# Kernel optimization log

Hardware: AMD Instinct MI355X
Metric: run time of the kernel (lower is better)

Reference implementation:

```python
import jax, jax.numpy as jnp
import numpy as np

B, T = 8192, 2048


def setup_inputs() -> dict:
    key = jax.random.key(0)
    u = jax.random.normal(key, (B, T, 1), dtype=jnp.float32)
    return {
        "u": u,
        "dt": jnp.float32(0.01),
        "m": jnp.float32(1.0),
        "c": jnp.float32(0.1),
        "k": jnp.float32(2.0),
        "in_mean": jnp.float32(0.5),
        "in_std": jnp.float32(2.0),
        "out_mean": jnp.float32(0.0),
        "out_std": jnp.float32(1.5),
    }


def reference(u, dt, m, c, k, in_mean, in_std, out_mean, out_std):
    # u: (B, T, 1) scaled forcing signal; state: (B, 2) = [position, velocity]
    Bsz = u.shape[0]
    u_seq = jnp.transpose(u[..., 0])  # (T, B) for lax.scan over time
    state0 = jnp.zeros((Bsz, 2), dtype=u.dtype)

    def step(state, u_t):
        # in_s.inverse_transform: unscale input
        u_p = u_t * in_std + in_mean  # (B,)
        x, v = state[:, 0], state[:, 1]
        # prior(state, u_p): mass-spring-damper derivative [dx, dv]
        acc = (u_p - c * v - k * x) / m
        new_state = state + dt * jnp.stack([v, acc], axis=1)  # Euler step
        # prior.ay on the UPDATED state (matches torch: state updated first)
        ay = (u_p - c * new_state[:, 1] - k * new_state[:, 0]) / m
        # out_s.transform: scale output
        y = (ay - out_mean) / out_std  # (B,)
        return new_state, y

    state_T, ys = jax.lax.scan(step, state0, u_seq)  # ys: (T, B)
    return jnp.transpose(ys), state_T  # (B, T), (B, 2)
```

## Files before the change

### kernel.cpp

```cpp
#include <hip/hip_runtime.h>

#define TT 2048

__device__ __forceinline__ float b2f(unsigned short h) {
    union { unsigned int u; float f; } x; x.u = ((unsigned int)h) << 16; return x.f;
}
__device__ __forceinline__ unsigned short f2b(float f) {
    union { float f; unsigned int u; } x; x.f = f;
    unsigned int r = x.u + 0x7fffu + ((x.u >> 16) & 1u);
    return (unsigned short)(r >> 16);
}
__device__ __forceinline__ float ldsc(const void* p, bool bf) {
    return bf ? b2f(*(const unsigned short*)p) : *(const float*)p;
}
__device__ __forceinline__ int swz(int u) { return u ^ ((u >> 3) & 7); }

__device__ __forceinline__ void gload16(const void* g, void* lds_base) {
    __builtin_amdgcn_global_load_lds(
        (const __attribute__((address_space(1))) void*)g,
        (__attribute__((address_space(3))) void*)lds_base,
        16, 0, 0);
}

template<bool BF>
__device__ __forceinline__ void issue_row_loads(const void* u_in, int r, int lane, uint4* Wb) {
    constexpr int NLD = BF ? 4 : 8;
    constexpr int ES  = BF ? 2 : 4;
    const char* g = (const char*)u_in + (size_t)r * TT * ES;
    #pragma unroll
    for (int j = 0; j < NLD; j++)
        gload16(g + (size_t)swz(j * 64 + lane) * 16, (char*)Wb + j * 1024);
}

template<bool BF>
__device__ void run_wave(
    const void* __restrict__ u_in, void* __restrict__ out,
    int rows, int row0, int stride, int lane,
    uint4* __restrict__ U0, uint4* __restrict__ U1,
    float dt, float cc, float kk, float inv_m,
    float im, float is, float om, float inv_os)
{
    constexpr int NLD = BF ? 4 : 8;
    constexpr int ES  = BF ? 2 : 4;

    const float a21 = -dt * kk * inv_m;
    const float a22 = 1.0f - dt * cc * inv_m;
    const float dtm = dt * inv_m;

    issue_row_loads<BF>(u_in, row0, lane, U0);

    int p = 0;
    bool first = true;
    for (int r = row0; r < rows; r += stride) {
        uint4* W  = p ? U1 : U0;
        uint4* Wn = p ? U0 : U1;

        if (first)      { asm volatile("s_waitcnt vmcnt(0)" ::: "memory"); }
        else if (BF)    { asm volatile("s_waitcnt vmcnt(5)" ::: "memory"); }
        else            { asm volatile("s_waitcnt vmcnt(9)" ::: "memory"); }
        __builtin_amdgcn_sched_barrier(0);

        const int rn = r + stride;
        if (rn < rows) issue_row_loads<BF>(u_in, rn, lane, Wn);
        __builtin_amdgcn_sched_barrier(0);

        float uf[32];
        if (BF) {
            #pragma unroll
            for (int m = 0; m < 4; m++) {
                uint4 w = W[swz(lane * 4 + m)];
                unsigned int ws[4] = {w.x, w.y, w.z, w.w};
                #pragma unroll
                for (int q = 0; q < 4; q++) {
                    uf[m*8 + q*2 + 0] = b2f((unsigned short)(ws[q] & 0xffffu));
                    uf[m*8 + q*2 + 1] = b2f((unsigned short)(ws[q] >> 16));
                }
            }
        } else {
            #pragma unroll
            for (int m = 0; m < 8; m++) {
                uint4 w = W[swz(lane * 8 + m)];
                uf[m*4+0] = __uint_as_float(w.x);
                uf[m*4+1] = __uint_as_float(w.y);
                uf[m*4+2] = __uint_as_float(w.z);
                uf[m*4+3] = __uint_as_float(w.w);
            }
        }

        float px = 0.f, pv = 0.f;
        #pragma unroll
        for (int i = 0; i < 32; i++) {
            float up = uf[i] * is + im;
            uf[i] = up;
            float nx = px + dt * pv;
            float nv = a21 * px + a22 * pv + dtm * up;
            px = nx; pv = nv;
        }

        float m00 = 1.f, m01 = dt, m10 = a21, m11 = a22;
        #pragma unroll
        for (int i = 0; i < 5; i++) {
            float t00 = m00*m00 + m01*m10;
            float t01 = m00*m01 + m01*m11;
            float t10 = m10*m00 + m11*m10;
            float t11 = m10*m01 + m11*m11;
            m00=t00; m01=t01; m10=t10; m11=t11;
        }

        #pragma unroll
        for (int o = 1; o < 64; o <<= 1) {
            float rx = __shfl_up(px, o, 64);
            float rv = __shfl_up(pv, o, 64);
            if (lane >= o) {
                px = m00*rx + m01*rv + px;
                pv = m10*rx + m11*rv + pv;
            }
            if (o < 32) {
                float t00 = m00*m00 + m01*m10;
                float t01 = m00*m01 + m01*m11;
                float t10 = m10*m00 + m11*m10;
                float t11 = m10*m01 + m11*m11;
                m00=t00; m01=t01; m10=t10; m11=t11;
            }
        }

        float ex = __shfl_up(px, 1, 64);
        float ev = __shfl_up(pv, 1, 64);
        if (lane == 0) { ex = 0.f; ev = 0.f; }

        float x = ex, v = ev;
        #pragma unroll
        for (int i = 0; i < 32; i++) {
            float up = uf[i];
            float nx = x + dt * v;
            float nv = a21 * x + a22 * v + dtm * up;
            float ay = (up - cc * nv - kk * nx) * inv_m;
            uf[i] = (ay - om) * inv_os;
            x = nx; v = nv;
        }

        if (BF) {
            #pragma unroll
            for (int m = 0; m < 4; m++) {
                uint4 w;
                w.x = (unsigned)f2b(uf[m*8+0]) | ((unsigned)f2b(uf[m*8+1]) << 16);
                w.y = (unsigned)f2b(uf[m*8+2]) | ((unsigned)f2b(uf[m*8+3]) << 16);
                w.z = (unsigned)f2b(uf[m*8+4]) | ((unsigned)f2b(uf[m*8+5]) << 16);
                w.w = (unsigned)f2b(uf[m*8+6]) | ((unsigned)f2b(uf[m*8+7]) << 16);
                W[swz(lane * 4 + m)] = w;
            }
        } else {
            #pragma unroll
            for (int m = 0; m < 8; m++) {
                uint4 w;
                w.x = __float_as_uint(uf[m*4+0]);
                w.y = __float_as_uint(uf[m*4+1]);
                w.z = __float_as_uint(uf[m*4+2]);
                w.w = __float_as_uint(uf[m*4+3]);
                W[swz(lane * 8 + m)] = w;
            }
        }
        __builtin_amdgcn_wave_barrier();

        {
            uint4* g = (uint4*)((char*)out + (size_t)r * TT * ES);
            #pragma unroll
            for (int j = 0; j < NLD; j++) g[j * 64 + lane] = W[swz(j * 64 + lane)];
        }
        if (lane == 63) {
            if (BF) {
                unsigned short* ob = (unsigned short*)out;
                size_t so = (size_t)rows * TT + (size_t)r * 2;
                *(unsigned int*)(ob + so) =
                    (unsigned)f2b(px) | ((unsigned)f2b(pv) << 16);
            } else {
                float* of = (float*)out;
                size_t so = (size_t)rows * TT + (size_t)r * 2;
                *(float2*)(of + so) = make_float2(px, pv);
            }
        }

        p ^= 1;
        first = false;
    }
}

__global__ __launch_bounds__(128, 2) void phys_scan(
    const void* __restrict__ u_in,
    const void* __restrict__ p_dt, const void* __restrict__ p_m,
    const void* __restrict__ p_c,  const void* __restrict__ p_k,
    const void* __restrict__ p_im, const void* __restrict__ p_is,
    const void* __restrict__ p_om, const void* __restrict__ p_os,
    void* __restrict__ out, int rows, int stride)
{
    __shared__ uint4 smem[2][2][512];
    const int lane = threadIdx.x & 63;
    const int wid  = threadIdx.x >> 6;
    const int row0 = blockIdx.x * 2 + wid;
    if (row0 >= rows) return;

    const bool bf = (((const unsigned short*)p_m)[0] != 0);

    const float dt = ldsc(p_dt, bf);
    const float mm = ldsc(p_m,  bf);
    const float cc = ldsc(p_c,  bf);
    const float kk = ldsc(p_k,  bf);
    const float im = ldsc(p_im, bf);
    const float is = ldsc(p_is, bf);
    const float om = ldsc(p_om, bf);
    const float os = ldsc(p_os, bf);
    const float inv_m  = 1.0f / mm;
    const float inv_os = 1.0f / os;

    if (bf) run_wave<true >(u_in, out, rows, row0, stride, lane,
                            smem[wid][0], smem[wid][1],
                            dt, cc, kk, inv_m, im, is, om, inv_os);
    else    run_wave<false>(u_in, out, rows, row0, stride, lane,
                            smem[wid][0], smem[wid][1],
                            dt, cc, kk, inv_m, im, is, om, inv_os);
}

extern "C" void kernel_launch(void* const* d_in, const int* in_sizes, int n_in,
                              void* d_out, int out_size, void* d_ws, size_t ws_size,
                              hipStream_t stream) {
    const int rows = in_sizes[0] / TT;
    int blocks = (rows + 1) / 2;
    if (blocks > 1024) blocks = 1024;
    const int stride = blocks * 2;
    hipLaunchKernelGGL(phys_scan, dim3(blocks), dim3(128), 0, stream,
                       d_in[0], d_in[1], d_in[2], d_in[3], d_in[4],
                       d_in[5], d_in[6], d_in[7], d_in[8],
                       d_out, rows, stride);
}
```

Before: 126.6 us.

## Prefetch rows into registers with a single LDS buffer and double the grid

Replaces the direct global-to-LDS async loads and the LDS double buffer with a register prefetch of the next row. That row is written into one swizzled LDS buffer at the start of each iteration. Halving LDS use allows launch bounds of 4 blocks per CU, and the launcher now allows up to 2048 blocks, so each wave handles fewer rows and more waves run concurrently. The trade-off is extra VGPRs for the prefetch registers. The hardcoded vmcnt waits also no longer match the new load pattern, so the compiler's own waits must preserve ordering.

```diff
diff --git a/kernel.cpp b/kernel.cpp
--- a/kernel.cpp
+++ b/kernel.cpp
@@ -15,28 +15,11 @@
 }
 __device__ __forceinline__ int swz(int u) { return u ^ ((u >> 3) & 7); }
 
-__device__ __forceinline__ void gload16(const void* g, void* lds_base) {
-    __builtin_amdgcn_global_load_lds(
-        (const __attribute__((address_space(1))) void*)g,
-        (__attribute__((address_space(3))) void*)lds_base,
-        16, 0, 0);
-}
-
-template<bool BF>
-__device__ __forceinline__ void issue_row_loads(const void* u_in, int r, int lane, uint4* Wb) {
-    constexpr int NLD = BF ? 4 : 8;
-    constexpr int ES  = BF ? 2 : 4;
-    const char* g = (const char*)u_in + (size_t)r * TT * ES;
-    #pragma unroll
-    for (int j = 0; j < NLD; j++)
-        gload16(g + (size_t)swz(j * 64 + lane) * 16, (char*)Wb + j * 1024);
-}
-
 template<bool BF>
 __device__ void run_wave(
     const void* __restrict__ u_in, void* __restrict__ out,
     int rows, int row0, int stride, int lane,
-    uint4* __restrict__ U0, uint4* __restrict__ U1,
+    uint4* __restrict__ W,
     float dt, float cc, float kk, float inv_m,
     float im, float is, float om, float inv_os)
 {
@@ -47,21 +30,29 @@
     const float a22 = 1.0f - dt * cc * inv_m;
     const float dtm = dt * inv_m;
 
-    issue_row_loads<BF>(u_in, row0, lane, U0);
-
-    int p = 0;
+    uint4 pf[NLD];
+    {
+        const uint4* g = (const uint4*)((const char*)u_in + (size_t)row0 * TT * ES);
+        #pragma unroll
+        for (int j = 0; j < NLD; j++) pf[j] = g[j * 64 + lane];
+    }
+
     bool first = true;
     for (int r = row0; r < rows; r += stride) {
-        uint4* W  = p ? U1 : U0;
-        uint4* Wn = p ? U0 : U1;
-
         if (first)      { asm volatile("s_waitcnt vmcnt(0)" ::: "memory"); }
         else if (BF)    { asm volatile("s_waitcnt vmcnt(5)" ::: "memory"); }
         else            { asm volatile("s_waitcnt vmcnt(9)" ::: "memory"); }
         __builtin_amdgcn_sched_barrier(0);
 
+        #pragma unroll
+        for (int j = 0; j < NLD; j++) W[swz(j * 64 + lane)] = pf[j];
+
         const int rn = r + stride;
-        if (rn < rows) issue_row_loads<BF>(u_in, rn, lane, Wn);
+        if (rn < rows) {
+            const uint4* g = (const uint4*)((const char*)u_in + (size_t)rn * TT * ES);
+            #pragma unroll
+            for (int j = 0; j < NLD; j++) pf[j] = g[j * 64 + lane];
+        }
         __builtin_amdgcn_sched_barrier(0);
 
         float uf[32];
@@ -165,7 +156,10 @@
         {
             uint4* g = (uint4*)((char*)out + (size_t)r * TT * ES);
             #pragma unroll
-            for (int j = 0; j < NLD; j++) g[j * 64 + lane] = W[swz(j * 64 + lane)];
+            for (int j = 0; j < NLD; j++) {
+                uint4 t = W[swz(j * 64 + lane)];
+                g[j * 64 + lane] = t;
+            }
         }
         if (lane == 63) {
             if (BF) {
@@ -180,12 +174,11 @@
             }
         }
 
-        p ^= 1;
         first = false;
     }
 }
 
-__global__ __launch_bounds__(128, 2) void phys_scan(
+__global__ __launch_bounds__(128, 4) void phys_scan(
     const void* __restrict__ u_in,
     const void* __restrict__ p_dt, const void* __restrict__ p_m,
     const void* __restrict__ p_c,  const void* __restrict__ p_k,
@@ -193,7 +186,7 @@
     const void* __restrict__ p_om, const void* __restrict__ p_os,
     void* __restrict__ out, int rows, int stride)
 {
-    __shared__ uint4 smem[2][2][512];
+    __shared__ uint4 smem[2][512];
     const int lane = threadIdx.x & 63;
     const int wid  = threadIdx.x >> 6;
     const int row0 = blockIdx.x * 2 + wid;
@@ -212,11 +205,9 @@
     const float inv_m  = 1.0f / mm;
     const float inv_os = 1.0f / os;
 
-    if (bf) run_wave<true >(u_in, out, rows, row0, stride, lane,
-                            smem[wid][0], smem[wid][1],
+    if (bf) run_wave<true >(u_in, out, rows, row0, stride, lane, smem[wid],
                             dt, cc, kk, inv_m, im, is, om, inv_os);
-    else    run_wave<false>(u_in, out, rows, row0, stride, lane,
-                            smem[wid][0], smem[wid][1],
+    else    run_wave<false>(u_in, out, rows, row0, stride, lane, smem[wid],
                             dt, cc, kk, inv_m, im, is, om, inv_os);
 }
 
@@ -224,8 +215,10 @@
                               void* d_out, int out_size, void* d_ws, size_t ws_size,
                               hipStream_t stream) {
     const int rows = in_sizes[0] / TT;
-    int blocks = (rows + 1) / 2;
-    if (blocks > 1024) blocks = 1024;
+    int waves = rows / 2;
+    if (waves < 1) waves = rows;
+    int blocks = (waves + 1) / 2;
+    if (blocks > 2048) blocks = 2048;
     const int stride = blocks * 2;
     hipLaunchKernelGGL(phys_scan, dim3(blocks), dim3(128), 0, stream,
                        d_in[0], d_in[1], d_in[2], d_in[3], d_in[4],
```

After: 202.8 us. +60.1%, slower.

## Split row staging into half-buffers and size grid so each wave handles two rows

Applied to the files above, without the earlier changes.

The per-wave LDS double buffer is replaced by two half-row buffers. The next row's first half is loaded as soon as the current first half has been read into registers, and its second half is loaded after the output staging through buffer B finishes. This halves LDS use per block, which allows more resident blocks, and the grid is now sized so each wave processes about two rows instead of capping at 1024 blocks. The cost is more waitcnt juggling, a second staging pass for output, and less prefetch distance per row.

```diff
diff --git a/kernel.cpp b/kernel.cpp
--- a/kernel.cpp
+++ b/kernel.cpp
@@ -23,12 +23,12 @@
 }
 
 template<bool BF>
-__device__ __forceinline__ void issue_row_loads(const void* u_in, int r, int lane, uint4* Wb) {
-    constexpr int NLD = BF ? 4 : 8;
-    constexpr int ES  = BF ? 2 : 4;
-    const char* g = (const char*)u_in + (size_t)r * TT * ES;
+__device__ __forceinline__ void issue_half(const void* u_in, int r, int h, int lane, uint4* Wb) {
+    constexpr int NH = BF ? 2 : 4;
+    constexpr int ES = BF ? 2 : 4;
+    const char* g = (const char*)u_in + (size_t)r * TT * ES + (size_t)h * (NH * 1024);
     #pragma unroll
-    for (int j = 0; j < NLD; j++)
+    for (int j = 0; j < NH; j++)
         gload16(g + (size_t)swz(j * 64 + lane) * 16, (char*)Wb + j * 1024);
 }
 
@@ -36,54 +36,95 @@
 __device__ void run_wave(
     const void* __restrict__ u_in, void* __restrict__ out,
     int rows, int row0, int stride, int lane,
-    uint4* __restrict__ U0, uint4* __restrict__ U1,
+    uint4* __restrict__ A, uint4* __restrict__ B,
     float dt, float cc, float kk, float inv_m,
     float im, float is, float om, float inv_os)
 {
-    constexpr int NLD = BF ? 4 : 8;
-    constexpr int ES  = BF ? 2 : 4;
+    constexpr int NH = BF ? 2 : 4;
+    constexpr int ES = BF ? 2 : 4;
+    constexpr int NU = BF ? 4 : 8;
 
     const float a21 = -dt * kk * inv_m;
     const float a22 = 1.0f - dt * cc * inv_m;
     const float dtm = dt * inv_m;
 
-    issue_row_loads<BF>(u_in, row0, lane, U0);
-
-    int p = 0;
+    issue_half<BF>(u_in, row0, 0, lane, A);
+    issue_half<BF>(u_in, row0, 1, lane, B);
+
     bool first = true;
     for (int r = row0; r < rows; r += stride) {
-        uint4* W  = p ? U1 : U0;
-        uint4* Wn = p ? U0 : U1;
-
-        if (first)      { asm volatile("s_waitcnt vmcnt(0)" ::: "memory"); }
-        else if (BF)    { asm volatile("s_waitcnt vmcnt(5)" ::: "memory"); }
-        else            { asm volatile("s_waitcnt vmcnt(9)" ::: "memory"); }
+        const int rn = r + stride;
+        const bool last = (rn >= rows);
+
+        if (first) {
+            if (BF) asm volatile("s_waitcnt vmcnt(2)"  ::: "memory");
+            else    asm volatile("s_waitcnt vmcnt(4)"  ::: "memory");
+        } else {
+            if (BF) asm volatile("s_waitcnt vmcnt(7)"  ::: "memory");
+            else    asm volatile("s_waitcnt vmcnt(13)" ::: "memory");
+        }
         __builtin_amdgcn_sched_barrier(0);
 
-        const int rn = r + stride;
-        if (rn < rows) issue_row_loads<BF>(u_in, rn, lane, Wn);
+        float uf[32];
+        if (lane < 32) {
+            if (BF) {
+                #pragma unroll
+                for (int m = 0; m < 4; m++) {
+                    uint4 w = A[swz(lane * 4 + m)];
+                    unsigned int ws[4] = {w.x, w.y, w.z, w.w};
+                    #pragma unroll
+                    for (int q = 0; q < 4; q++) {
+                        uf[m*8 + q*2 + 0] = b2f((unsigned short)(ws[q] & 0xffffu));
+                        uf[m*8 + q*2 + 1] = b2f((unsigned short)(ws[q] >> 16));
+                    }
+                }
+            } else {
+                #pragma unroll
+                for (int m = 0; m < 8; m++) {
+                    uint4 w = A[swz(lane * 8 + m)];
+                    uf[m*4+0] = __uint_as_float(w.x);
+                    uf[m*4+1] = __uint_as_float(w.y);
+                    uf[m*4+2] = __uint_as_float(w.z);
+                    uf[m*4+3] = __uint_as_float(w.w);
+                }
+            }
+        }
+        asm volatile("s_waitcnt lgkmcnt(0)" ::: "memory");
         __builtin_amdgcn_sched_barrier(0);
 
-        float uf[32];
-        if (BF) {
-            #pragma unroll
-            for (int m = 0; m < 4; m++) {
-                uint4 w = W[swz(lane * 4 + m)];
-                unsigned int ws[4] = {w.x, w.y, w.z, w.w};
-                #pragma unroll
-                for (int q = 0; q < 4; q++) {
-                    uf[m*8 + q*2 + 0] = b2f((unsigned short)(ws[q] & 0xffffu));
-                    uf[m*8 + q*2 + 1] = b2f((unsigned short)(ws[q] >> 16));
-                }
-            }
+        if (!last) issue_half<BF>(u_in, rn, 0, lane, A);
+        __builtin_amdgcn_sched_barrier(0);
+
+        if (last) {
+            asm volatile("s_waitcnt vmcnt(0)" ::: "memory");
+        } else if (BF) {
+            asm volatile("s_waitcnt vmcnt(2)" ::: "memory");
         } else {
-            #pragma unroll
-            for (int m = 0; m < 8; m++) {
-                uint4 w = W[swz(lane * 8 + m)];
-                uf[m*4+0] = __uint_as_float(w.x);
-                uf[m*4+1] = __uint_as_float(w.y);
-                uf[m*4+2] = __uint_as_float(w.z);
-                uf[m*4+3] = __uint_as_float(w.w);
+            asm volatile("s_waitcnt vmcnt(4)" ::: "memory");
+        }
+        __builtin_amdgcn_sched_barrier(0);
+
+        if (lane >= 32) {
+            if (BF) {
+                #pragma unroll
+                for (int m = 0; m < 4; m++) {
+                    uint4 w = B[swz((lane - 32) * 4 + m)];
+                    unsigned int ws[4] = {w.x, w.y, w.z, w.w};
+                    #pragma unroll
+                    for (int q = 0; q < 4; q++) {
+                        uf[m*8 + q*2 + 0] = b2f((unsigned short)(ws[q] & 0xffffu));
+                        uf[m*8 + q*2 + 1] = b2f((unsigned short)(ws[q] >> 16));
+                    }
+                }
+            } else {
+                #pragma unroll
+                for (int m = 0; m < 8; m++) {
+                    uint4 w = B[swz((lane - 32) * 8 + m)];
+                    uf[m*4+0] = __uint_as_float(w.x);
+                    uf[m*4+1] = __uint_as_float(w.y);
+                    uf[m*4+2] = __uint_as_float(w.z);
+                    uf[m*4+3] = __uint_as_float(w.w);
+                }
             }
         }
 
@@ -139,33 +180,66 @@
             x = nx; v = nv;
         }
 
-        if (BF) {
-            #pragma unroll
-            for (int m = 0; m < 4; m++) {
-                uint4 w;
-                w.x = (unsigned)f2b(uf[m*8+0]) | ((unsigned)f2b(uf[m*8+1]) << 16);
-                w.y = (unsigned)f2b(uf[m*8+2]) | ((unsigned)f2b(uf[m*8+3]) << 16);
-                w.z = (unsigned)f2b(uf[m*8+4]) | ((unsigned)f2b(uf[m*8+5]) << 16);
-                w.w = (unsigned)f2b(uf[m*8+6]) | ((unsigned)f2b(uf[m*8+7]) << 16);
-                W[swz(lane * 4 + m)] = w;
-            }
-        } else {
-            #pragma unroll
-            for (int m = 0; m < 8; m++) {
-                uint4 w;
-                w.x = __float_as_uint(uf[m*4+0]);
-                w.y = __float_as_uint(uf[m*4+1]);
-                w.z = __float_as_uint(uf[m*4+2]);
-                w.w = __float_as_uint(uf[m*4+3]);
-                W[swz(lane * 8 + m)] = w;
+        uint4* g = (uint4*)((char*)out + (size_t)r * TT * ES);
+        if (lane < 32) {
+            if (BF) {
+                #pragma unroll
+                for (int m = 0; m < 4; m++) {
+                    uint4 w;
+                    w.x = (unsigned)f2b(uf[m*8+0]) | ((unsigned)f2b(uf[m*8+1]) << 16);
+                    w.y = (unsigned)f2b(uf[m*8+2]) | ((unsigned)f2b(uf[m*8+3]) << 16);
+                    w.z = (unsigned)f2b(uf[m*8+4]) | ((unsigned)f2b(uf[m*8+5]) << 16);
+                    w.w = (unsigned)f2b(uf[m*8+6]) | ((unsigned)f2b(uf[m*8+7]) << 16);
+                    B[swz(lane * 4 + m)] = w;
+                }
+            } else {
+                #pragma unroll
+                for (int m = 0; m < 8; m++) {
+                    uint4 w;
+                    w.x = __float_as_uint(uf[m*4+0]);
+                    w.y = __float_as_uint(uf[m*4+1]);
+                    w.z = __float_as_uint(uf[m*4+2]);
+                    w.w = __float_as_uint(uf[m*4+3]);
+                    B[swz(lane * 8 + m)] = w;
+                }
             }
         }
         __builtin_amdgcn_wave_barrier();
-
-        {
-            uint4* g = (uint4*)((char*)out + (size_t)r * TT * ES);
-            #pragma unroll
-            for (int j = 0; j < NLD; j++) g[j * 64 + lane] = W[swz(j * 64 + lane)];
+        #pragma unroll
+        for (int j = 0; j < NH; j++) {
+            uint4 t = B[swz(j * 64 + lane)];
+            g[j * 64 + lane] = t;
+        }
+        __builtin_amdgcn_wave_barrier();
+
+        if (lane >= 32) {
+            if (BF) {
+                #pragma unroll
+                for (int m = 0; m < 4; m++) {
+                    uint4 w;
+                    w.x = (unsigned)f2b(uf[m*8+0]) | ((unsigned)f2b(uf[m*8+1]) << 16);
+                    w.y = (unsigned)f2b(uf[m*8+2]) | ((unsigned)f2b(uf[m*8+3]) << 16);
+                    w.z = (unsigned)f2b(uf[m*8+4]) | ((unsigned)f2b(uf[m*8+5]) << 16);
+                    w.w = (unsigned)f2b(uf[m*8+6]) | ((unsigned)f2b(uf[m*8+7]) << 16);
+                    B[swz((lane - 32) * 4 + m)] = w;
+                }
+            } else {
+                #pragma unroll
+                for (int m = 0; m < 8; m++) {
+                    uint4 w;
+                    w.x = __float_as_uint(uf[m*4+0]);
+                    w.y = __float_as_uint(uf[m*4+1]);
+                    w.z = __float_as_uint(uf[m*4+2]);
+                    w.w = __float_as_uint(uf[m*4+3]);
+                    B[swz((lane - 32) * 8 + m)] = w;
+                }
+            }
+        }
+        __builtin_amdgcn_wave_barrier();
+        #pragma unroll
+        for (int j = 0; j < NH; j++) {
+            uint4 t = B[swz(j * 64 + lane)];
+            g[(NH + j) * 64 + lane] = t;
         }
         if (lane == 63) {
             if (BF) {
@@ -179,8 +253,10 @@
                 *(float2*)(of + so) = make_float2(px, pv);
             }
         }
-
-        p ^= 1;
+        __builtin_amdgcn_wave_barrier();
+
+        if (!last) issue_half<BF>(u_in, rn, 1, lane, B);
+
         first = false;
     }
 }
@@ -193,7 +269,7 @@
     const void* __restrict__ p_om, const void* __restrict__ p_os,
     void* __restrict__ out, int rows, int stride)
 {
-    __shared__ uint4 smem[2][2][512];
+    __shared__ uint4 smem[2][2][256];
     const int lane = threadIdx.x & 63;
     const int wid  = threadIdx.x >> 6;
     const int row0 = blockIdx.x * 2 + wid;
@@ -224,8 +300,9 @@
                               void* d_out, int out_size, void* d_ws, size_t ws_size,
                               hipStream_t stream) {
     const int rows = in_sizes[0] / TT;
-    int blocks = (rows + 1) / 2;
-    if (blocks > 1024) blocks = 1024;
+    int waves = (rows + 1) / 2;
+    int blocks = (waves + 1) / 2;
+    if (blocks < 1) blocks = 1;
     const int stride = blocks * 2;
     hipLaunchKernelGGL(phys_scan, dim3(blocks), dim3(128), 0, stream,
                        d_in[0], d_in[1], d_in[2], d_in[3], d_in[4],
```

After: 129.8 us. 1.03x slower.
